# Performance work log

Measured on AMD Instinct MI355X. Metric: run time of the kernel, lower is better.

Reference implementation:

```python
import math
import jax, jax.numpy as jnp
import numpy as np

FACTOR = 2  # init kwarg of AutoCorrelation


def setup_inputs() -> dict:
    key0 = jax.random.key(0)
    kq, kk, kv = jax.random.split(key0, 3)
    B, H, L, D = 8, 8, 2048, 64
    return {
        "query": jax.random.normal(kq, (B, H, L, D), dtype=jnp.float32),
        "key": jax.random.normal(kk, (B, H, L, D), dtype=jnp.float32),
        "value": jax.random.normal(kv, (B, H, L, D), dtype=jnp.float32),
    }


def reference(query, key, value):
    # Inference (eval-mode) path of AutoCorrelation.forward.
    B, H, L, D = query.shape
    L_KV = key.shape[2]
    # _pad_or_truncate_key_value: match key/value length to query length
    if L > L_KV:
        pad = [(0, 0), (0, 0), (0, L - L_KV), (0, 0)]
        key = jnp.pad(key, pad)
        value = jnp.pad(value, pad)
    else:
        key = key[:, :, :L, :]
        value = value[:, :, :L, :]

    # _period_based_dependency: circular cross-correlation via FFT
    qf = jnp.fft.rfft(jnp.swapaxes(query, -2, -1), axis=-1)   # (B,H,D,L//2+1) complex
    kf = jnp.fft.rfft(jnp.swapaxes(key, -2, -1), axis=-1)
    corr = jnp.fft.irfft(qf * jnp.conj(kf), n=L, axis=-1)     # (B,H,D,L)

    # _time_delay_aggregation (eval branch: per-batch topk delays)
    mean_corr = corr.mean(axis=(1, 2))                         # (B,L)
    num_delays = min(FACTOR * math.ceil(math.log(L)), L)
    w, delay_idx = jax.lax.top_k(mean_corr, num_delays)       # (B,k)
    w = jax.nn.softmax(w, axis=-1)

    ar = jnp.arange(L)

    def body(ctx, inp):
        d, wk = inp  # (B,), (B,)
        idx = (ar[None, :] + d[:, None]) % L                   # (B,L) — circular shift == gather from doubled value
        gathered = jnp.take_along_axis(
            value, jnp.broadcast_to(idx[:, None, :, None], value.shape), axis=2
        )                                                      # (B,H,L,D)
        return ctx + wk[:, None, None, None] * gathered, None

    ctx0 = jnp.zeros_like(value)
    context, _ = jax.lax.scan(body, ctx0, (delay_idx.T, w.T))
    return context
```

## Files before the change

### kernel.cpp

```cpp
#include <hip/hip_runtime.h>

static constexpr int LSEQ = 2048;
static constexpr int NB   = 8;
static constexpr int NH   = 8;
static constexpr int ND   = 64;
static constexpr int NDEL = 16;

static constexpr size_t WS_P_OFF     = 0;
static constexpr size_t WS_W_OFF     = 8388608;
static constexpr size_t WS_DELAY_OFF = 8389120;

__device__ __forceinline__ int SWZ(int x) { return x ^ (((x >> 4) & 7) << 1); }

__device__ __forceinline__ int pof(int f) {
    return ((f & 7) << 8) | (((f >> 3) & 7) << 5) | (((f >> 6) & 7) << 2) | (f >> 9);
}
__device__ __forceinline__ int fofp(int p) {
    return (p >> 8) | (((p >> 5) & 7) << 3) | (((p >> 2) & 7) << 6) | ((p & 3) << 9);
}

#define CMUL(ar, ai, br, bi) make_float2((ar)*(br) - (ai)*(bi), (ar)*(bi) + (ai)*(br))

__device__ __forceinline__ void dft8(const float2 x[8], float2 X[8]) {
    const float RH = 0.70710678118654752440f;
    float2 a0 = make_float2(x[0].x + x[4].x, x[0].y + x[4].y);
    float2 a1 = make_float2(x[1].x + x[5].x, x[1].y + x[5].y);
    float2 a2 = make_float2(x[2].x + x[6].x, x[2].y + x[6].y);
    float2 a3 = make_float2(x[3].x + x[7].x, x[3].y + x[7].y);
    float2 b0 = make_float2(x[0].x - x[4].x, x[0].y - x[4].y);
    float  t1r = x[1].x - x[5].x, t1i = x[1].y - x[5].y;
    float2 b1 = make_float2(RH * (t1r + t1i), RH * (t1i - t1r));
    float  t2r = x[2].x - x[6].x, t2i = x[2].y - x[6].y;
    float2 b2 = make_float2(t2i, -t2r);
    float  t3r = x[3].x - x[7].x, t3i = x[3].y - x[7].y;
    float2 b3 = make_float2(RH * (t3i - t3r), -RH * (t3r + t3i));
    float2 c0 = make_float2(a0.x + a2.x, a0.y + a2.y);
    float2 d0 = make_float2(a0.x - a2.x, a0.y - a2.y);
    float2 c1 = make_float2(a1.x + a3.x, a1.y + a3.y);
    float2 d1 = make_float2(a1.y - a3.y, -(a1.x - a3.x));
    X[0] = make_float2(c0.x + c1.x, c0.y + c1.y);
    X[4] = make_float2(c0.x - c1.x, c0.y - c1.y);
    X[2] = make_float2(d0.x + d1.x, d0.y + d1.y);
    X[6] = make_float2(d0.x - d1.x, d0.y - d1.y);
    float2 e0 = make_float2(b0.x + b2.x, b0.y + b2.y);
    float2 f0 = make_float2(b0.x - b2.x, b0.y - b2.y);
    float2 e1 = make_float2(b1.x + b3.x, b1.y + b3.y);
    float2 f1 = make_float2(b1.y - b3.y, -(b1.x - b3.x));
    X[1] = make_float2(e0.x + e1.x, e0.y + e1.y);
    X[5] = make_float2(e0.x - e1.x, e0.y - e1.y);
    X[3] = make_float2(f0.x + f1.x, f0.y + f1.y);
    X[7] = make_float2(f0.x - f1.x, f0.y - f1.y);
}

__device__ __forceinline__ void dft4(const float2 x[4], float2 X[4]) {
    float2 s0 = make_float2(x[0].x + x[2].x, x[0].y + x[2].y);
    float2 s1 = make_float2(x[1].x + x[3].x, x[1].y + x[3].y);
    float2 d0 = make_float2(x[0].x - x[2].x, x[0].y - x[2].y);
    float2 d1 = make_float2(x[1].y - x[3].y, -(x[1].x - x[3].x));
    X[0] = make_float2(s0.x + s1.x, s0.y + s1.y);
    X[2] = make_float2(s0.x - s1.x, s0.y - s1.y);
    X[1] = make_float2(d0.x + d1.x, d0.y + d1.y);
    X[3] = make_float2(d0.x - d1.x, d0.y - d1.y);
}

__device__ __forceinline__ void stageR8(float2* zp, const int adr[8], const float2 W[7]) {
    float2 X[8], Y[8];
    #pragma unroll
    for (int j = 0; j < 8; ++j) X[j] = zp[adr[j]];
    dft8(X, Y);
    #pragma unroll
    for (int m = 1; m < 8; ++m) Y[m] = CMUL(Y[m].x, Y[m].y, W[m-1].x, W[m-1].y);
    #pragma unroll
    for (int m = 0; m < 8; ++m) zp[adr[m]] = Y[m];
}

__device__ __forceinline__ void stageD(float2* zp, const int adr[8], float2 X[8]) {
    float2 xin[8];
    #pragma unroll
    for (int j = 0; j < 8; ++j) xin[j] = zp[adr[j]];
    dft4(&xin[0], &X[0]);
    dft4(&xin[4], &X[4]);
    #pragma unroll
    for (int m = 0; m < 8; ++m) zp[adr[m]] = X[m];
}

__global__ __launch_bounds__(256, 2) void fft_corr(const float* __restrict__ q,
                                                   const float* __restrict__ k,
                                                   float2* __restrict__ P) {
    __shared__ float2 z0[LSEQ], z1[LSEQ];
    const int t   = threadIdx.x;
    const int bi  = blockIdx.x;
    const int xcd = bi & 7;
    const int sl  = bi >> 3;
    const int bh  = xcd * 8 + (sl >> 3);
    const int grp = sl & 7;
    const int b   = bh >> 3;
    const int h   = bh & 7;
    const size_t base = (size_t)bh * LSEQ * ND + (size_t)(grp * 8);

    float2 WA[7], WB[7], WC[7];
    {
        float sn, cs;
        __sincosf(-6.28318530717958647692f * (float)t / 2048.f, &sn, &cs);
        WA[0] = make_float2(cs, sn);
        __sincosf(-6.28318530717958647692f * (float)(t & 31) / 256.f, &sn, &cs);
        WB[0] = make_float2(cs, sn);
        __sincosf(-6.28318530717958647692f * (float)(t & 3) / 32.f, &sn, &cs);
        WC[0] = make_float2(cs, sn);
        #pragma unroll
        for (int m = 1; m < 7; ++m) {
            WA[m] = CMUL(WA[m-1].x, WA[m-1].y, WA[0].x, WA[0].y);
            WB[m] = CMUL(WB[m-1].x, WB[m-1].y, WB[0].x, WB[0].y);
            WC[m] = CMUL(WC[m-1].x, WC[m-1].y, WC[0].x, WC[0].y);
        }
    }

    int fS[4], pmS[4];
    #pragma unroll
    for (int s = 0; s < 4; ++s) {
        const int cc = (s < 2) ? s : s + 2;
        const int f  = fofp(8 * t + cc);
        const int m  = (2048 - f) & 2047;
        fS[s]  = f;
        pmS[s] = SWZ(pof(m));
    }
    float aFr[4] = {0, 0, 0, 0}, aFi[4] = {0, 0, 0, 0};
    float aS = 0.f;

    const int sbB   = (t >> 5) * 256 + (t & 31);
    const int baseC = (t >> 2) * 32 + (t & 3);
    int adrB[8], adrC[8], adrD[8];
    #pragma unroll
    for (int n = 0; n < 8; ++n) {
        adrB[n] = SWZ(sbB + 32 * n);
        adrC[n] = SWZ(baseC + 4 * n);
        adrD[n] = SWZ(8 * t + n);
    }

    #pragma unroll
    for (int half = 0; half < 2; ++half) {
        float4 qa[8], ka[8];
        #pragma unroll
        for (int j = 0; j < 8; ++j) {
            const size_t r = base + (size_t)(t + 256 * j) * ND + half * 4;
            qa[j] = *(const float4*)(q + r);
            ka[j] = *(const float4*)(k + r);
        }
        #pragma unroll
        for (int pr = 0; pr < 2; ++pr) {
            const int c0 = 2 * pr, c1 = 2 * pr + 1;
            float2 X0[8], X1[8], Y0[8], Y1[8];
            #pragma unroll
            for (int j = 0; j < 8; ++j) {
                X0[j] = make_float2((&qa[j].x)[c0], (&ka[j].x)[c0]);
                X1[j] = make_float2((&qa[j].x)[c1], (&ka[j].x)[c1]);
            }
            __syncthreads();

            dft8(X0, Y0);
            dft8(X1, Y1);
            #pragma unroll
            for (int m = 1; m < 8; ++m) {
                Y0[m] = CMUL(Y0[m].x, Y0[m].y, WA[m-1].x, WA[m-1].y);
                Y1[m] = CMUL(Y1[m].x, Y1[m].y, WA[m-1].x, WA[m-1].y);
            }
            #pragma unroll
            for (int m = 0; m < 8; ++m) {
                const int a = SWZ(m * 256 + t);
                z0[a] = Y0[m];
                z1[a] = Y1[m];
            }
            __syncthreads();

            stageR8(z0, adrB, WB);
            stageR8(z1, adrB, WB);
            __syncthreads();

            stageR8(z0, adrC, WC);
            stageR8(z1, adrC, WC);
            __syncthreads();

            stageD(z0, adrD, X0);
            stageD(z1, adrD, X1);
            __syncthreads();

            #pragma unroll
            for (int s = 0; s < 4; ++s) {
                const int cc = (s < 2) ? s : s + 2;
                {
                    const float2 Zf = X0[cc], Zm = z0[pmS[s]];
                    const float qr = 0.5f * (Zf.x + Zm.x), qi = 0.5f * (Zf.y - Zm.y);
                    const float kr = 0.5f * (Zf.y + Zm.y), ki = 0.5f * (Zm.x - Zf.x);
                    aFr[s] += qr * kr + qi * ki;
                    aFi[s] += qi * kr - qr * ki;
                }
                {
                    const float2 Zf = X1[cc], Zm = z1[pmS[s]];
                    const float qr = 0.5f * (Zf.x + Zm.x), qi = 0.5f * (Zf.y - Zm.y);
                    const float kr = 0.5f * (Zf.y + Zm.y), ki = 0.5f * (Zm.x - Zf.x);
                    aFr[s] += qr * kr + qi * ki;
                    aFi[s] += qi * kr - qr * ki;
                }
            }
            if (t == 0) aS += X0[2].x * X0[2].y + X1[2].x * X1[2].y;
        }
    }

    const int part = h * 8 + grp;
    float2* Pp = P + (size_t)part * (NB * 2048) + (size_t)b * 2048;
    *(float4*)&Pp[8 * t]     = make_float4(aFr[0], aFi[0], aFr[1], aFi[1]);
    *(float4*)&Pp[8 * t + 4] = make_float4(aFr[2], aFi[2], aFr[3], aFi[3]);
    #pragma unroll
    for (int s = 0; s < 4; ++s) {
        const int m = (2048 - fS[s]) & 2047;
        if (m != fS[s]) Pp[pof(m)] = make_float2(aFr[s], -aFi[s]);
    }
    if (t == 0) Pp[pof(1024)] = make_float2(aS, 0.f);
}

__global__ __launch_bounds__(256) void reduce_S(float2* __restrict__ P) {
    const int g = blockIdx.x * 256 + threadIdx.x;
    float ax = 0.f, ay = 0.f;
    #pragma unroll 8
    for (int part = 0; part < 64; ++part) {
        const float2 v = P[(size_t)part * (NB * 2048) + g];
        ax += v.x; ay += v.y;
    }
    P[g] = make_float2(ax, ay);
}

__global__ __launch_bounds__(256) void ifft_topk(const float2* __restrict__ S,
                                                 float* __restrict__ wout,
                                                 int* __restrict__ dout) {
    __shared__ float2 zz[LSEQ];
    __shared__ float  mc[LSEQ];
    __shared__ float  pv[4];
    __shared__ int    pig[4];
    __shared__ float  topv[NDEL];
    __shared__ int    topi[NDEL];
    const int b = blockIdx.x, t = threadIdx.x;

    float2 WA[7], WB[7], WC[7];
    {
        float sn, cs;
        __sincosf(-6.28318530717958647692f * (float)t / 2048.f, &sn, &cs);
        WA[0] = make_float2(cs, sn);
        __sincosf(-6.28318530717958647692f * (float)(t & 31) / 256.f, &sn, &cs);
        WB[0] = make_float2(cs, sn);
        __sincosf(-6.28318530717958647692f * (float)(t & 3) / 32.f, &sn, &cs);
        WC[0] = make_float2(cs, sn);
        #pragma unroll
        for (int m = 1; m < 7; ++m) {
            WA[m] = CMUL(WA[m-1].x, WA[m-1].y, WA[0].x, WA[0].y);
            WB[m] = CMUL(WB[m-1].x, WB[m-1].y, WB[0].x, WB[0].y);
            WC[m] = CMUL(WC[m-1].x, WC[m-1].y, WC[0].x, WC[0].y);
        }
    }
    const int sbB   = (t >> 5) * 256 + (t & 31);
    const int baseC = (t >> 2) * 32 + (t & 3);
    int adrB[8], adrC[8], adrD[8];
    #pragma unroll
    for (int n = 0; n < 8; ++n) {
        adrB[n] = SWZ(sbB + 32 * n);
        adrC[n] = SWZ(baseC + 4 * n);
        adrD[n] = SWZ(8 * t + n);
    }

    #pragma unroll
    for (int j = 0; j < 8; ++j) zz[t + 256 * j] = S[b * 2048 + t + 256 * j];
    __syncthreads();

    float2 X[8], Y[8];
    #pragma unroll
    for (int j = 0; j < 8; ++j) {
        const float2 s = zz[pof(t + 256 * j)];
        X[j] = make_float2(s.x, -s.y);
    }
    __syncthreads();

    dft8(X, Y);
    #pragma unroll
    for (int m = 1; m < 8; ++m) Y[m] = CMUL(Y[m].x, Y[m].y, WA[m-1].x, WA[m-1].y);
    #pragma unroll
    for (int m = 0; m < 8; ++m) zz[SWZ(m * 256 + t)] = Y[m];
    __syncthreads();

    stageR8(zz, adrB, WB);
    __syncthreads();
    stageR8(zz, adrC, WC);
    __syncthreads();

    {
        float2 xin[8];
        #pragma unroll
        for (int j = 0; j < 8; ++j) xin[j] = zz[adrD[j]];
        dft4(&xin[0], &X[0]);
        dft4(&xin[4], &X[4]);
    }

    const float scale = 1.0f / ((float)LSEQ * (float)(NH * ND));
    #pragma unroll
    for (int cc = 0; cc < 8; ++cc) mc[fofp(8 * t + cc)] = X[cc].x * scale;
    __syncthreads();

    const int lane = t & 63, wv = t >> 6;
    for (int it = 0; it < NDEL; ++it) {
        float bv = -3e38f; int bix = 0;
        #pragma unroll
        for (int u = 0; u < 8; ++u) {
            const int idx = t + 256 * u;
            const float v = mc[idx];
            if (v > bv || (v == bv && idx < bix)) { bv = v; bix = idx; }
        }
        #pragma unroll
        for (int off = 32; off; off >>= 1) {
            const float ov = __shfl_xor(bv, off);
            const int   oi = __shfl_xor(bix, off);
            if (ov > bv || (ov == bv && oi < bix)) { bv = ov; bix = oi; }
        }
        if (lane == 0) { pv[wv] = bv; pig[wv] = bix; }
        __syncthreads();
        if (t < 64) {
            float v = (t < 4) ? pv[t] : -3e38f;
            int  ii = (t < 4) ? pig[t] : 0;
            #pragma unroll
            for (int off = 2; off; off >>= 1) {
                const float ov = __shfl_xor(v, off);
                const int   oi = __shfl_xor(ii, off);
                if (ov > v || (ov == v && oi < ii)) { v = ov; ii = oi; }
            }
            if (t == 0) { topv[it] = v; topi[it] = ii; mc[ii] = -3e38f; }
        }
        __syncthreads();
    }

    if (t == 0) {
        const float m = topv[0];
        float e[NDEL], sum = 0.f;
        for (int i = 0; i < NDEL; ++i) { e[i] = __expf(topv[i] - m); sum += e[i]; }
        const float inv = 1.0f / sum;
        for (int i = 0; i < NDEL; ++i) {
            wout[b * NDEL + i] = e[i] * inv;
            dout[b * NDEL + i] = topi[i];
        }
    }
}

__global__ __launch_bounds__(256) void gather_out(const float* __restrict__ v,
                                                  const float* __restrict__ w,
                                                  const int* __restrict__ delay,
                                                  float* __restrict__ out) {
    const int bi  = blockIdx.x;
    const int xcd = bi & 7;
    const int s   = bi >> 3;
    const int bh  = xcd * 8 + (s >> 7);
    const int bt  = s & 127;
    const int b   = bh >> 3;
    const int tid = threadIdx.x;

    __shared__ float sw_[NDEL];
    __shared__ int   sd_[NDEL];
    if (tid < NDEL) {
        sw_[tid] = w[b * NDEL + tid];
        sd_[tid] = delay[b * NDEL + tid];
    }
    __syncthreads();

    const float* vb = v + (size_t)bh * LSEQ * ND;
    float*       ob = out + (size_t)bh * LSEQ * ND;

    const int row = tid >> 4;
    const int col = (tid & 15) * 4;
    const int t   = bt * 16 + row;

    float4 acc = make_float4(0.f, 0.f, 0.f, 0.f);
    #pragma unroll
    for (int kk = 0; kk < NDEL; ++kk) {
        const int r = (t + sd_[kk]) & (LSEQ - 1);
        const float4 vv = *(const float4*)(vb + (size_t)r * ND + col);
        const float wv = sw_[kk];
        acc.x += wv * vv.x; acc.y += wv * vv.y;
        acc.z += wv * vv.z; acc.w += wv * vv.w;
    }
    *(float4*)(ob + (size_t)t * ND + col) = acc;
}

extern "C" void kernel_launch(void* const* d_in, const int* in_sizes, int n_in,
                              void* d_out, int out_size, void* d_ws, size_t ws_size,
                              hipStream_t stream) {
    const float* q = (const float*)d_in[0];
    const float* k = (const float*)d_in[1];
    const float* v = (const float*)d_in[2];
    float* out = (float*)d_out;

    float2* P     = (float2*)((char*)d_ws + WS_P_OFF);
    float*  w     = (float*)((char*)d_ws + WS_W_OFF);
    int*    delay = (int*)((char*)d_ws + WS_DELAY_OFF);

    fft_corr<<<dim3(512), dim3(256), 0, stream>>>(q, k, P);
    reduce_S<<<dim3(64), dim3(256), 0, stream>>>(P);
    ifft_topk<<<dim3(NB), dim3(256), 0, stream>>>(P, w, delay);
    gather_out<<<dim3(NB * NH * 128), dim3(256), 0, stream>>>(v, w, delay, out);
}
```

Measured before the change: 200.2 us.

## Batch four FFT columns per barrier and use barrier-free per-wave top-k

The correlation FFT kernel now keeps four columns in shared memory at once (32 KB more LDS) and runs each radix stage across all four before each barrier. This halves the number of __syncthreads per half and drops the register copies of the final stage, which are now read back from LDS. The top-k kernel keeps candidates in registers and runs 16 wave-local argmax rounds without block barriers, then one wave merges the 64 candidates. The cost is higher LDS use in fft_corr, which may reduce occupancy, and the half loop is no longer unrolled.

```diff
diff --git a/kernel.cpp b/kernel.cpp
--- a/kernel.cpp
+++ b/kernel.cpp
@@ -74,8 +74,8 @@
     for (int m = 0; m < 8; ++m) zp[adr[m]] = Y[m];
 }
 
-__device__ __forceinline__ void stageD(float2* zp, const int adr[8], float2 X[8]) {
-    float2 xin[8];
+__device__ __forceinline__ void stageD4(float2* zp, const int adr[8]) {
+    float2 xin[8], X[8];
     #pragma unroll
     for (int j = 0; j < 8; ++j) xin[j] = zp[adr[j]];
     dft4(&xin[0], &X[0]);
@@ -87,7 +87,7 @@
 __global__ __launch_bounds__(256, 2) void fft_corr(const float* __restrict__ q,
                                                    const float* __restrict__ k,
                                                    float2* __restrict__ P) {
-    __shared__ float2 z0[LSEQ], z1[LSEQ];
+    __shared__ float2 zP[4][LSEQ];
     const int t   = threadIdx.x;
     const int bi  = blockIdx.x;
     const int xcd = bi & 7;
@@ -137,7 +137,7 @@
         adrD[n] = SWZ(8 * t + n);
     }
 
-    #pragma unroll
+    #pragma unroll 1
     for (int half = 0; half < 2; ++half) {
         float4 qa[8], ka[8];
         #pragma unroll
@@ -146,63 +146,54 @@
             qa[j] = *(const float4*)(q + r);
             ka[j] = *(const float4*)(k + r);
         }
-        #pragma unroll
-        for (int pr = 0; pr < 2; ++pr) {
-            const int c0 = 2 * pr, c1 = 2 * pr + 1;
-            float2 X0[8], X1[8], Y0[8], Y1[8];
-            #pragma unroll
-            for (int j = 0; j < 8; ++j) {
-                X0[j] = make_float2((&qa[j].x)[c0], (&ka[j].x)[c0]);
-                X1[j] = make_float2((&qa[j].x)[c1], (&ka[j].x)[c1]);
+        __syncthreads();
+
+        #pragma unroll
+        for (int c = 0; c < 4; ++c) {
+            float2 X[8], Y[8];
+            #pragma unroll
+            for (int j = 0; j < 8; ++j)
+                X[j] = make_float2((&qa[j].x)[c], (&ka[j].x)[c]);
+            dft8(X, Y);
+            #pragma unroll
+            for (int m = 1; m < 8; ++m) Y[m] = CMUL(Y[m].x, Y[m].y, WA[m-1].x, WA[m-1].y);
+            #pragma unroll
+            for (int m = 0; m < 8; ++m) zP[c][SWZ(m * 256 + t)] = Y[m];
+        }
+        __syncthreads();
+
+        #pragma unroll
+        for (int c = 0; c < 4; ++c) stageR8(zP[c], adrB, WB);
+        __syncthreads();
+
+        #pragma unroll
+        for (int c = 0; c < 4; ++c) stageR8(zP[c], adrC, WC);
+        __syncthreads();
+
+        #pragma unroll
+        for (int c = 0; c < 4; ++c) stageD4(zP[c], adrD);
+        __syncthreads();
+
+        #pragma unroll
+        for (int s = 0; s < 4; ++s) {
+            const int cc = (s < 2) ? s : s + 2;
+            const int own = adrD[cc];
+            #pragma unroll
+            for (int c = 0; c < 4; ++c) {
+                const float2 Zf = zP[c][own];
+                const float2 Zm = zP[c][pmS[s]];
+                const float qr = 0.5f * (Zf.x + Zm.x), qi = 0.5f * (Zf.y - Zm.y);
+                const float kr = 0.5f * (Zf.y + Zm.y), ki = 0.5f * (Zm.x - Zf.x);
+                aFr[s] += qr * kr + qi * ki;
+                aFi[s] += qi * kr - qr * ki;
             }
-            __syncthreads();
-
-            dft8(X0, Y0);
-            dft8(X1, Y1);
-            #pragma unroll
-            for (int m = 1; m < 8; ++m) {
-                Y0[m] = CMUL(Y0[m].x, Y0[m].y, WA[m-1].x, WA[m-1].y);
-                Y1[m] = CMUL(Y1[m].x, Y1[m].y, WA[m-1].x, WA[m-1].y);
+        }
+        if (t == 0) {
+            #pragma unroll
+            for (int c = 0; c < 4; ++c) {
+                const float2 Z = zP[c][adrD[2]];
+                aS += Z.x * Z.y;
             }
-            #pragma unroll
-            for (int m = 0; m < 8; ++m) {
-                const int a = SWZ(m * 256 + t);
-                z0[a] = Y0[m];
-                z1[a] = Y1[m];
-            }
-            __syncthreads();
-
-            stageR8(z0, adrB, WB);
-            stageR8(z1, adrB, WB);
-            __syncthreads();
-
-            stageR8(z0, adrC, WC);
-            stageR8(z1, adrC, WC);
-            __syncthreads();
-
-            stageD(z0, adrD, X0);
-            stageD(z1, adrD, X1);
-            __syncthreads();
-
-            #pragma unroll
-            for (int s = 0; s < 4; ++s) {
-                const int cc = (s < 2) ? s : s + 2;
-                {
-                    const float2 Zf = X0[cc], Zm = z0[pmS[s]];
-                    const float qr = 0.5f * (Zf.x + Zm.x), qi = 0.5f * (Zf.y - Zm.y);
-                    const float kr = 0.5f * (Zf.y + Zm.y), ki = 0.5f * (Zm.x - Zf.x);
-                    aFr[s] += qr * kr + qi * ki;
-                    aFi[s] += qi * kr - qr * ki;
-                }
-                {
-                    const float2 Zf = X1[cc], Zm = z1[pmS[s]];
-                    const float qr = 0.5f * (Zf.x + Zm.x), qi = 0.5f * (Zf.y - Zm.y);
-                    const float kr = 0.5f * (Zf.y + Zm.y), ki = 0.5f * (Zm.x - Zf.x);
-                    aFr[s] += qr * kr + qi * ki;
-                    aFi[s] += qi * kr - qr * ki;
-                }
-            }
-            if (t == 0) aS += X0[2].x * X0[2].y + X1[2].x * X1[2].y;
         }
     }
 
@@ -233,12 +224,12 @@
                                                  float* __restrict__ wout,
                                                  int* __restrict__ dout) {
     __shared__ float2 zz[LSEQ];
-    __shared__ float  mc[LSEQ];
-    __shared__ float  pv[4];
-    __shared__ int    pig[4];
+    __shared__ float  candV[64];
+    __shared__ int    candI[64];
     __shared__ float  topv[NDEL];
     __shared__ int    topi[NDEL];
     const int b = blockIdx.x, t = threadIdx.x;
+    const int lane = t & 63, wv = t >> 6;
 
     float2 WA[7], WB[7], WC[7];
     {
@@ -290,58 +281,63 @@
     stageR8(zz, adrC, WC);
     __syncthreads();
 
+    float vreg[8]; int ireg[8];
     {
         float2 xin[8];
         #pragma unroll
         for (int j = 0; j < 8; ++j) xin[j] = zz[adrD[j]];
         dft4(&xin[0], &X[0]);
         dft4(&xin[4], &X[4]);
-    }
-
-    const float scale = 1.0f / ((float)LSEQ * (float)(NH * ND));
-    #pragma unroll
-    for (int cc = 0; cc < 8; ++cc) mc[fofp(8 * t + cc)] = X[cc].x * scale;
-    __syncthreads();
-
-    const int lane = t & 63, wv = t >> 6;
+        const float scale = 1.0f / ((float)LSEQ * (float)(NH * ND));
+        #pragma unroll
+        for (int cc = 0; cc < 8; ++cc) {
+            vreg[cc] = X[cc].x * scale;
+            ireg[cc] = fofp(8 * t + cc);
+        }
+    }
+
     for (int it = 0; it < NDEL; ++it) {
-        float bv = -3e38f; int bix = 0;
-        #pragma unroll
-        for (int u = 0; u < 8; ++u) {
-            const int idx = t + 256 * u;
-            const float v = mc[idx];
-            if (v > bv || (v == bv && idx < bix)) { bv = v; bix = idx; }
-        }
+        float bv = -3e38f; int bix = 0x7fffffff, bcc = -1;
+        #pragma unroll
+        for (int cc = 0; cc < 8; ++cc) {
+            if (vreg[cc] > bv || (vreg[cc] == bv && ireg[cc] < bix)) {
+                bv = vreg[cc]; bix = ireg[cc]; bcc = cc;
+            }
+        }
+        float fv = bv; int fix = bix;
         #pragma unroll
         for (int off = 32; off; off >>= 1) {
-            const float ov = __shfl_xor(bv, off);
-            const int   oi = __shfl_xor(bix, off);
-            if (ov > bv || (ov == bv && oi < bix)) { bv = ov; bix = oi; }
-        }
-        if (lane == 0) { pv[wv] = bv; pig[wv] = bix; }
-        __syncthreads();
-        if (t < 64) {
-            float v = (t < 4) ? pv[t] : -3e38f;
-            int  ii = (t < 4) ? pig[t] : 0;
-            #pragma unroll
-            for (int off = 2; off; off >>= 1) {
-                const float ov = __shfl_xor(v, off);
-                const int   oi = __shfl_xor(ii, off);
-                if (ov > v || (ov == v && oi < ii)) { v = ov; ii = oi; }
+            const float ov = __shfl_xor(fv, off);
+            const int   oi = __shfl_xor(fix, off);
+            if (ov > fv || (ov == fv && oi < fix)) { fv = ov; fix = oi; }
+        }
+        if (fix == bix && bcc >= 0) vreg[bcc] = -3e38f;
+        if (lane == 0) { candV[wv * NDEL + it] = fv; candI[wv * NDEL + it] = fix; }
+    }
+    __syncthreads();
+
+    if (wv == 0) {
+        float val = candV[lane]; int idx = candI[lane];
+        for (int it = 0; it < NDEL; ++it) {
+            float fv = val; int fix = idx;
+            #pragma unroll
+            for (int off = 32; off; off >>= 1) {
+                const float ov = __shfl_xor(fv, off);
+                const int   oi = __shfl_xor(fix, off);
+                if (ov > fv || (ov == fv && oi < fix)) { fv = ov; fix = oi; }
             }
-            if (t == 0) { topv[it] = v; topi[it] = ii; mc[ii] = -3e38f; }
-        }
-        __syncthreads();
-    }
-
-    if (t == 0) {
-        const float m = topv[0];
-        float e[NDEL], sum = 0.f;
-        for (int i = 0; i < NDEL; ++i) { e[i] = __expf(topv[i] - m); sum += e[i]; }
-        const float inv = 1.0f / sum;
-        for (int i = 0; i < NDEL; ++i) {
-            wout[b * NDEL + i] = e[i] * inv;
-            dout[b * NDEL + i] = topi[i];
+            if (idx == fix) val = -3e38f;
+            if (lane == 0) { topv[it] = fv; topi[it] = fix; }
+        }
+        if (lane == 0) {
+            const float m = topv[0];
+            float e[NDEL], sum = 0.f;
+            for (int i = 0; i < NDEL; ++i) { e[i] = __expf(topv[i] - m); sum += e[i]; }
+            const float inv = 1.0f / sum;
+            for (int i = 0; i < NDEL; ++i) {
+                wout[b * NDEL + i] = e[i] * inv;
+                dout[b * NDEL + i] = topi[i];
+            }
         }
     }
 }
```

Measured after the change: 209.8 us. 4.8% more time.
